# Kernel optimization log

Hardware: AMD Instinct MI355X
Metric: run time of the kernel (lower is better)

Reference implementation:

```python
import jax, jax.numpy as jnp
import numpy as np

B, L, V = 8192, 64, 28
LATENT = 32
PAD_TOKEN, EOS_TOKEN = 26, 27
EPS = 1e-7
LETTER_FREQS = jnp.array([0.0817, 0.0149, 0.0278, 0.0425, 0.127, 0.0223, 0.0202,
                          0.0609, 0.0697, 0.0015, 0.0077, 0.0403, 0.0241, 0.0675,
                          0.0751, 0.0193, 0.001, 0.0599, 0.0633, 0.0906, 0.0276,
                          0.0098, 0.0236, 0.0015, 0.0197, 0.0007], dtype=jnp.float32)
FREQS_PAD = jnp.pad(LETTER_FREQS, (0, V - 26))  # tf.pad to VOCAB_SIZE


def setup_inputs() -> dict:
    key = jax.random.key(0)
    k1, k2, k3, k4, k5 = jax.random.split(key, 5)
    x = jax.random.normal(k1, (B, L, V), dtype=jnp.float32)
    # decoder output is a softmax -> valid probability tensor
    reconstruction = jax.nn.softmax(jax.random.normal(k2, (B, L, V), dtype=jnp.float32), axis=-1)
    z_mean = jax.random.normal(k3, (B, LATENT), dtype=jnp.float32)
    z_log_var = jax.random.normal(k4, (B, LATENT), dtype=jnp.float32)
    classifier_score = jax.random.uniform(k5, (B, 1), dtype=jnp.float32)
    return {"x": x, "reconstruction": reconstruction, "z_mean": z_mean,
            "z_log_var": z_log_var, "classifier_score": classifier_score}


def _total_loss(x, reconstruction, z_mean, z_log_var, classifier_score):
    targets = jnp.argmax(x, axis=-1)                       # [B, L] int
    mask = (targets != PAD_TOKEN).astype(jnp.float32)      # [B, L]

    # sparse categorical CE on probabilities (tf clips probs)
    p_tgt = jnp.take_along_axis(reconstruction, targets[..., None], axis=-1)[..., 0]
    per_position_loss = -jnp.log(jnp.clip(p_tgt, EPS, 1.0))
    reconstruction_loss = jnp.sum(per_position_loss * mask) / jnp.sum(mask)

    kl_loss = -0.5 * jnp.mean(1.0 + z_log_var - jnp.square(z_mean) - jnp.exp(z_log_var))

    classifier_loss = -jnp.mean(jnp.log(classifier_score + EPS))

    # consecutive similarity: sum_i i^2.5 * sum_j prod(adjacent[:, j:j+i])
    mask_adj = (targets[:, 1:] != PAD_TOKEN).astype(jnp.float32)       # [B, L-1]
    adjacent = jnp.sum(reconstruction[:, 1:] * reconstruction[:, :-1], axis=-1) * mask_adj
    Lm1 = L - 1
    pos = jnp.arange(Lm1)

    def step(carry, k):
        # k = i - 1; p[:, j] holds prod(adjacent[:, j:j+k]) from previous step
        p, acc = carry
        valid = (pos < (Lm1 - k)).astype(adjacent.dtype)               # [L-1]
        shifted = jnp.roll(adjacent, -k, axis=1) * valid               # adjacent[:, j+k], 0 past end
        p = p * shifted                                                # window length k+1; invalid j -> 0
        w = jnp.power((k + 1).astype(jnp.float32), 2.5)
        acc = acc + w * jnp.sum(p)
        return (p, acc), None

    init = (adjacent, jnp.sum(adjacent))                               # i = 1, weight 1^2.5
    (_, consecutive_similarity), _ = jax.lax.scan(step, init, jnp.arange(1, Lm1))

    mask_exp = jnp.logical_and(targets != PAD_TOKEN, targets != EOS_TOKEN).astype(jnp.float32)[:, :, None]
    mean_letter_probs = jnp.sum(reconstruction * mask_exp, axis=(0, 1)) / jnp.sum(mask_exp)
    frequency_penalty = jnp.sum(jnp.maximum(0.0, mean_letter_probs - FREQS_PAD))

    total_loss = (reconstruction_loss + 0.1 * kl_loss + 2.0 * classifier_loss
                  + 0.2 * consecutive_similarity + 0.5 * frequency_penalty)
    return total_loss


def reference(x, reconstruction, z_mean, z_log_var, classifier_score):
    return _total_loss(x, reconstruction, z_mean, z_log_var, classifier_score)
```

## Files before the change

kernel.cpp:

```cpp
#include <hip/hip_runtime.h>
#include <math.h>

#define VB 28
#define LL 64
#define PAD_TOK 26
#define EOS_TOK 27
#define NSLOT 34
#define REPL 16
#define RPW 2

constexpr double csqrt_(double x) {
  double g = x > 1.0 ? x : 1.0;
  for (int i = 0; i < 60; ++i) g = 0.5 * (g + x / g);
  return g;
}
struct WTab { float w[64]; };
constexpr WTab make_wtab() {
  WTab t{};
  for (int k = 0; k < 64; ++k) {
    double n = (double)(k + 1);
    t.w[k] = (float)(n * n * csqrt_(n));
  }
  return t;
}
constexpr WTab WTAB = make_wtab();

__device__ __forceinline__ float wave_red(float v) {
  #pragma unroll
  for (int o = 32; o > 0; o >>= 1) v += __shfl_down(v, o, 64);
  return v;
}

__global__ __launch_bounds__(256) void vae_main(
    const float* __restrict__ x, const float* __restrict__ rec,
    const float* __restrict__ zm, const float* __restrict__ zlv,
    const float* __restrict__ cs, float* __restrict__ ws,
    int nrows, int nz, int nc, int nblocks) {
  __shared__ float adj_s[4][128];
  __shared__ float red[4][NSLOT];
  __shared__ float tr[4][64 * 29];
  const int lane = threadIdx.x & 63;
  const int wid  = threadIdx.x >> 6;
  adj_s[wid][64 + lane] = 0.f;
  __builtin_amdgcn_wave_barrier();

  float loss_acc = 0.f, mask_cnt = 0.f, mexp_cnt = 0.f;
  float consec0 = 0.f, consec1 = 0.f;
  float vocab[VB];
  #pragma unroll
  for (int v = 0; v < VB; ++v) vocab[v] = 0.f;

  const int wave_id = blockIdx.x * 4 + wid;
  const int row0 = wave_id * RPW;

  float4 xa[7], ra[7];
  {
    const int row = row0;
    if (row < nrows) {
      const size_t base = ((size_t)row * LL + lane) * VB;
      const float4* xp = reinterpret_cast<const float4*>(x + base);
      const float4* rp = reinterpret_cast<const float4*>(rec + base);
      #pragma unroll
      for (int i = 0; i < 7; ++i) { xa[i] = xp[i]; ra[i] = rp[i]; }
    }
  }

  #pragma unroll
  for (int it = 0; it < RPW; ++it) {
    const int row = row0 + it;
    if (row >= nrows) break;

    float4 xb[7], rb[7];
    const int nrow = row + 1;
    const bool pf = (it + 1 < RPW) && (nrow < nrows);
    if (pf) {
      const size_t base = ((size_t)nrow * LL + lane) * VB;
      const float4* xp = reinterpret_cast<const float4*>(x + base);
      const float4* rp = reinterpret_cast<const float4*>(rec + base);
      #pragma unroll
      for (int i = 0; i < 7; ++i) { xb[i] = xp[i]; rb[i] = rp[i]; }
    }

    float r[VB];
    float best = -INFINITY, pt = 0.f;
    int tgt = 0;
    #pragma unroll
    for (int i = 0; i < 7; ++i) {
      const float4 xq = xa[i];
      const float4 rq = ra[i];
      r[i*4+0] = rq.x; r[i*4+1] = rq.y; r[i*4+2] = rq.z; r[i*4+3] = rq.w;
      if (xq.x > best) { best = xq.x; tgt = i*4+0; pt = rq.x; }
      if (xq.y > best) { best = xq.y; tgt = i*4+1; pt = rq.y; }
      if (xq.z > best) { best = xq.z; tgt = i*4+2; pt = rq.z; }
      if (xq.w > best) { best = xq.w; tgt = i*4+3; pt = rq.w; }
    }
    const float mask = (tgt != PAD_TOK) ? 1.f : 0.f;
    const float mexp = (tgt != PAD_TOK && tgt != EOS_TOK) ? 1.f : 0.f;
    loss_acc += -__logf(fminf(fmaxf(pt, 1e-7f), 1.f)) * mask;
    mask_cnt += mask;
    mexp_cnt += mexp;
    #pragma unroll
    for (int v = 0; v < VB; ++v) vocab[v] += r[v] * mexp;

    float adj = 0.f;
    #pragma unroll
    for (int v = 0; v < VB; ++v) adj += r[v] * __shfl_down(r[v], 1, 64);
    const int tgt_next = __shfl_down(tgt, 1, 64);
    adj = (lane < 63 && tgt_next != PAD_TOK) ? adj : 0.f;

    __builtin_amdgcn_wave_barrier();
    adj_s[wid][lane] = adj;
    __builtin_amdgcn_wave_barrier();

    const float* ap = &adj_s[wid][lane];
    float p = adj;
    consec0 += p;
    #pragma unroll
    for (int k = 1; k <= 62; k += 2) {
      p *= ap[k];
      consec1 += WTAB.w[k] * p;
      if (k + 1 <= 62) {
        p *= ap[k + 1];
        consec0 += WTAB.w[k + 1] * p;
      }
    }
    __builtin_amdgcn_wave_barrier();

    if (pf) {
      #pragma unroll
      for (int i = 0; i < 7; ++i) { xa[i] = xb[i]; ra[i] = rb[i]; }
    }
  }
  float consec_acc = consec0 + consec1;

  const int gid = blockIdx.x * 256 + threadIdx.x;
  const int gstride = nblocks * 256;
  float kl = 0.f, cl = 0.f;
  for (int i = gid; i < nz; i += gstride) {
    const float m = zm[i], lv = zlv[i];
    kl += 1.f + lv - m * m - __expf(lv);
  }
  for (int i = gid; i < nc; i += gstride) cl += __logf(cs[i] + 1e-7f);

  loss_acc   = wave_red(loss_acc);
  mask_cnt   = wave_red(mask_cnt);
  consec_acc = wave_red(consec_acc);
  mexp_cnt   = wave_red(mexp_cnt);
  kl         = wave_red(kl);
  cl         = wave_red(cl);

  float* tw = &tr[wid][0];
  __builtin_amdgcn_wave_barrier();
  #pragma unroll
  for (int v = 0; v < VB; ++v) tw[lane * 29 + v] = vocab[v];
  __builtin_amdgcn_wave_barrier();
  float vs = 0.f;
  if (lane < VB) {
    float s0 = 0.f, s1 = 0.f, s2 = 0.f, s3 = 0.f;
    #pragma unroll
    for (int pidx = 0; pidx < 64; pidx += 4) {
      s0 += tw[(pidx + 0) * 29 + lane];
      s1 += tw[(pidx + 1) * 29 + lane];
      s2 += tw[(pidx + 2) * 29 + lane];
      s3 += tw[(pidx + 3) * 29 + lane];
    }
    vs = (s0 + s1) + (s2 + s3);
  }
  __builtin_amdgcn_wave_barrier();

  if (lane == 0) {
    red[wid][0] = loss_acc; red[wid][1] = mask_cnt;
    red[wid][2] = consec_acc; red[wid][3] = mexp_cnt;
    red[wid][4] = kl; red[wid][5] = cl;
  }
  if (lane < VB) red[wid][6 + lane] = vs;
  __syncthreads();
  if (threadIdx.x < NSLOT) {
    const int t = threadIdx.x;
    const int b = blockIdx.x & (REPL - 1);
    atomicAdd(&ws[t * (REPL * 32) + b * 32],
              red[0][t] + red[1][t] + red[2][t] + red[3][t]);
  }
}

__global__ void vae_finalize(const float* __restrict__ ws, float* __restrict__ out,
                             float nz, float nc) {
  if (threadIdx.x == 0 && blockIdx.x == 0) {
    const float freqs[VB] = {0.0817f,0.0149f,0.0278f,0.0425f,0.127f,0.0223f,
      0.0202f,0.0609f,0.0697f,0.0015f,0.0077f,0.0403f,0.0241f,0.0675f,0.0751f,
      0.0193f,0.001f,0.0599f,0.0633f,0.0906f,0.0276f,0.0098f,0.0236f,0.0015f,
      0.0197f,0.0007f,0.f,0.f};
    float fin[NSLOT];
    #pragma unroll
    for (int t = 0; t < NSLOT; ++t) {
      float s = 0.f;
      #pragma unroll
      for (int b = 0; b < REPL; ++b) s += ws[t * (REPL * 32) + b * 32];
      fin[t] = s;
    }
    const float rec_loss = fin[0] / fin[1];
    const float kl_loss  = -0.5f * fin[4] / nz;
    const float cls_loss = -fin[5] / nc;
    const float inv_mexp = 1.f / fin[3];
    float fp = 0.f;
    #pragma unroll
    for (int v = 0; v < VB; ++v)
      fp += fmaxf(0.f, fin[6 + v] * inv_mexp - freqs[v]);
    out[0] = rec_loss + 0.1f * kl_loss + 2.f * cls_loss
           + 0.2f * fin[2] + 0.5f * fp;
  }
}

extern "C" void kernel_launch(void* const* d_in, const int* in_sizes, int n_in,
                              void* d_out, int out_size, void* d_ws, size_t ws_size,
                              hipStream_t stream) {
  const float* x   = (const float*)d_in[0];
  const float* rec = (const float*)d_in[1];
  const float* zm  = (const float*)d_in[2];
  const float* zlv = (const float*)d_in[3];
  const float* cs  = (const float*)d_in[4];
  float* out = (float*)d_out;
  float* ws  = (float*)d_ws;

  const int nrows = in_sizes[0] / (LL * VB);
  const int nz    = in_sizes[2];
  const int nc    = in_sizes[4];

  int nblocks = (nrows + 4 * RPW - 1) / (4 * RPW);
  if (nblocks < 1) nblocks = 1;

  hipMemsetAsync(d_ws, 0, NSLOT * REPL * 32 * sizeof(float), stream);
  vae_main<<<nblocks, 256, 0, stream>>>(x, rec, zm, zlv, cs, ws,
                                        nrows, nz, nc, nblocks);
  vae_finalize<<<1, 64, 0, stream>>>(ws, out, (float)nz, (float)nc);
}
```

Measured before the change: 160.8 us.

## Deepen row prefetch to two-ahead and replace neighbour shuffles with LDS reads

Each wave now processes four rows instead of two, with a two-deep register double buffer, so loads for row+2 are issued while row+1's data is already resident. The 28 per-element cross-lane shuffles for the adjacent-position dot product are replaced by writing each position's reconstruction row into padded LDS and reading the neighbour's row from there. Targets are shared through LDS as well. Launch bounds now request two blocks per SM to cap registers. This trades shuffle cost for LDS traffic and uses more registers for the deeper prefetch, while halving the grid size.

```diff
diff --git a/kernel.cpp b/kernel.cpp
--- a/kernel.cpp
+++ b/kernel.cpp
@@ -7,7 +7,8 @@
 #define EOS_TOK 27
 #define NSLOT 34
 #define REPL 16
-#define RPW 2
+#define RPW 4
+#define RSTRIDE 29
 
 constexpr double csqrt_(double x) {
   double g = x > 1.0 ? x : 1.0;
@@ -31,14 +32,15 @@
   return v;
 }
 
-__global__ __launch_bounds__(256) void vae_main(
+__global__ __launch_bounds__(256, 2) void vae_main(
     const float* __restrict__ x, const float* __restrict__ rec,
     const float* __restrict__ zm, const float* __restrict__ zlv,
     const float* __restrict__ cs, float* __restrict__ ws,
     int nrows, int nz, int nc, int nblocks) {
+  __shared__ float row_s[4][65 * RSTRIDE];
   __shared__ float adj_s[4][128];
   __shared__ float red[4][NSLOT];
-  __shared__ float tr[4][64 * 29];
+  __shared__ int   tgt_s[4][64];
   const int lane = threadIdx.x & 63;
   const int wid  = threadIdx.x >> 6;
   adj_s[wid][64 + lane] = 0.f;
@@ -53,15 +55,16 @@
   const int wave_id = blockIdx.x * 4 + wid;
   const int row0 = wave_id * RPW;
 
-  float4 xa[7], ra[7];
-  {
-    const int row = row0;
+  float4 xb[2][7], rb[2][7];
+  #pragma unroll
+  for (int q = 0; q < 2; ++q) {
+    const int row = row0 + q;
     if (row < nrows) {
       const size_t base = ((size_t)row * LL + lane) * VB;
       const float4* xp = reinterpret_cast<const float4*>(x + base);
       const float4* rp = reinterpret_cast<const float4*>(rec + base);
       #pragma unroll
-      for (int i = 0; i < 7; ++i) { xa[i] = xp[i]; ra[i] = rp[i]; }
+      for (int i = 0; i < 7; ++i) { xb[q][i] = xp[i]; rb[q][i] = rp[i]; }
     }
   }
 
@@ -69,44 +72,51 @@
   for (int it = 0; it < RPW; ++it) {
     const int row = row0 + it;
     if (row >= nrows) break;
-
-    float4 xb[7], rb[7];
-    const int nrow = row + 1;
-    const bool pf = (it + 1 < RPW) && (nrow < nrows);
-    if (pf) {
-      const size_t base = ((size_t)nrow * LL + lane) * VB;
-      const float4* xp = reinterpret_cast<const float4*>(x + base);
-      const float4* rp = reinterpret_cast<const float4*>(rec + base);
-      #pragma unroll
-      for (int i = 0; i < 7; ++i) { xb[i] = xp[i]; rb[i] = rp[i]; }
-    }
-
-    float r[VB];
+    const int cur = it & 1;
+
     float best = -INFINITY, pt = 0.f;
     int tgt = 0;
     #pragma unroll
     for (int i = 0; i < 7; ++i) {
-      const float4 xq = xa[i];
-      const float4 rq = ra[i];
-      r[i*4+0] = rq.x; r[i*4+1] = rq.y; r[i*4+2] = rq.z; r[i*4+3] = rq.w;
+      const float4 xq = xb[cur][i];
+      const float4 rq = rb[cur][i];
+      row_s[wid][lane * RSTRIDE + i*4 + 0] = rq.x;
+      row_s[wid][lane * RSTRIDE + i*4 + 1] = rq.y;
+      row_s[wid][lane * RSTRIDE + i*4 + 2] = rq.z;
+      row_s[wid][lane * RSTRIDE + i*4 + 3] = rq.w;
       if (xq.x > best) { best = xq.x; tgt = i*4+0; pt = rq.x; }
       if (xq.y > best) { best = xq.y; tgt = i*4+1; pt = rq.y; }
       if (xq.z > best) { best = xq.z; tgt = i*4+2; pt = rq.z; }
       if (xq.w > best) { best = xq.w; tgt = i*4+3; pt = rq.w; }
     }
+    tgt_s[wid][lane] = tgt;
+    __builtin_amdgcn_wave_barrier();
+
+    if (it + 2 < RPW && row + 2 < nrows) {
+      const size_t base = ((size_t)(row + 2) * LL + lane) * VB;
+      const float4* xp = reinterpret_cast<const float4*>(x + base);
+      const float4* rp = reinterpret_cast<const float4*>(rec + base);
+      #pragma unroll
+      for (int i = 0; i < 7; ++i) { xb[cur][i] = xp[i]; rb[cur][i] = rp[i]; }
+    }
+
     const float mask = (tgt != PAD_TOK) ? 1.f : 0.f;
     const float mexp = (tgt != PAD_TOK && tgt != EOS_TOK) ? 1.f : 0.f;
     loss_acc += -__logf(fminf(fmaxf(pt, 1e-7f), 1.f)) * mask;
     mask_cnt += mask;
     mexp_cnt += mexp;
-    #pragma unroll
-    for (int v = 0; v < VB; ++v) vocab[v] += r[v] * mexp;
-
+
+    const float* own = &row_s[wid][lane * RSTRIDE];
+    const float* nbr = own + RSTRIDE;
     float adj = 0.f;
     #pragma unroll
-    for (int v = 0; v < VB; ++v) adj += r[v] * __shfl_down(r[v], 1, 64);
-    const int tgt_next = __shfl_down(tgt, 1, 64);
-    adj = (lane < 63 && tgt_next != PAD_TOK) ? adj : 0.f;
+    for (int v = 0; v < VB; ++v) {
+      const float ov = own[v];
+      vocab[v] += ov * mexp;
+      adj += ov * nbr[v];
+    }
+    const int tgtn = (lane < 63) ? tgt_s[wid][lane + 1] : PAD_TOK;
+    adj = (lane < 63 && tgtn != PAD_TOK) ? adj : 0.f;
 
     __builtin_amdgcn_wave_barrier();
     adj_s[wid][lane] = adj;
@@ -125,11 +135,6 @@
       }
     }
     __builtin_amdgcn_wave_barrier();
-
-    if (pf) {
-      #pragma unroll
-      for (int i = 0; i < 7; ++i) { xa[i] = xb[i]; ra[i] = rb[i]; }
-    }
   }
   float consec_acc = consec0 + consec1;
 
@@ -149,20 +154,20 @@
   kl         = wave_red(kl);
   cl         = wave_red(cl);
 
-  float* tw = &tr[wid][0];
-  __builtin_amdgcn_wave_barrier();
-  #pragma unroll
-  for (int v = 0; v < VB; ++v) tw[lane * 29 + v] = vocab[v];
+  float* tw = &row_s[wid][0];
+  __builtin_amdgcn_wave_barrier();
+  #pragma unroll
+  for (int v = 0; v < VB; ++v) tw[lane * RSTRIDE + v] = vocab[v];
   __builtin_amdgcn_wave_barrier();
   float vs = 0.f;
   if (lane < VB) {
     float s0 = 0.f, s1 = 0.f, s2 = 0.f, s3 = 0.f;
     #pragma unroll
     for (int pidx = 0; pidx < 64; pidx += 4) {
-      s0 += tw[(pidx + 0) * 29 + lane];
-      s1 += tw[(pidx + 1) * 29 + lane];
-      s2 += tw[(pidx + 2) * 29 + lane];
-      s3 += tw[(pidx + 3) * 29 + lane];
+      s0 += tw[(pidx + 0) * RSTRIDE + lane];
+      s1 += tw[(pidx + 1) * RSTRIDE + lane];
+      s2 += tw[(pidx + 2) * RSTRIDE + lane];
+      s3 += tw[(pidx + 3) * RSTRIDE + lane];
     }
     vs = (s0 + s1) + (s2 + s3);
   }
```

After: 161.4 us. Within noise of the previous version (+0.4%).
